# Kernel optimization log

Measured on AMD Instinct MI355X. Metric: run time of the kernel, lower is better.

## Reference

```python
import jax, jax.numpy as jnp
import numpy as np

B, N, D, H, DFF = 2, 2048, 1024, 16, 4096
HD = D // H
L = 3
WINDOWS = (256, 64, 16)   # sliding-window size per hierarchy level
LEVEL_SCALE = 16          # pos_l = token_idx // LEVEL_SCALE**l
EPS = 1e-5
NEG = -1e9


def setup_inputs() -> dict:
    key = jax.random.key(0)
    ks = jax.random.split(key, 16)
    s = 0.02
    x = jax.random.normal(ks[0], (B, N, D), dtype=jnp.float32)
    idx = jnp.arange(N, dtype=jnp.int32)
    positions = jnp.stack([idx // (LEVEL_SCALE ** l) for l in range(L)], axis=0)  # [L, N]
    return {
        "x": x,
        "positions": positions,
        "w_qkv": jax.random.normal(ks[1], (D, 3 * D), dtype=jnp.float32) * s,
        "b_qkv": jnp.zeros((3 * D,), dtype=jnp.float32),
        "w_out": jax.random.normal(ks[2], (D, D), dtype=jnp.float32) * s,
        "b_out": jnp.zeros((D,), dtype=jnp.float32),
        "w_ff1": jax.random.normal(ks[3], (D, DFF), dtype=jnp.float32) * s,
        "b_ff1": jnp.zeros((DFF,), dtype=jnp.float32),
        "w_ff2": jax.random.normal(ks[4], (DFF, D), dtype=jnp.float32) * s,
        "b_ff2": jnp.zeros((D,), dtype=jnp.float32),
        "g1": jnp.ones((D,), dtype=jnp.float32),
        "beta1": jnp.zeros((D,), dtype=jnp.float32),
        "g2": jnp.ones((D,), dtype=jnp.float32),
        "beta2": jnp.zeros((D,), dtype=jnp.float32),
    }


def _layernorm(x, g, b):
    m = jnp.mean(x, axis=-1, keepdims=True)
    v = jnp.var(x, axis=-1, keepdims=True)
    return (x - m) * jax.lax.rsqrt(v + EPS) * g + b


def _mlswa_mask(positions):
    # union over levels of per-level sliding windows: |pos_l[i]-pos_l[j]| < w_l
    allowed = jnp.zeros((N, N), dtype=bool)
    for l, w in enumerate(WINDOWS):
        p = positions[l]
        allowed = allowed | (jnp.abs(p[:, None] - p[None, :]) < w)
    return allowed  # [N, N]


def reference(x, positions, w_qkv, b_qkv, w_out, b_out,
              w_ff1, b_ff1, w_ff2, b_ff2, g1, beta1, g2, beta2):
    residual = x
    xn = _layernorm(x, g1, beta1)
    qkv = xn @ w_qkv + b_qkv                       # [B, N, 3D]
    qkv = qkv.reshape(B, N, 3, H, HD)
    q, k, v = qkv[:, :, 0], qkv[:, :, 1], qkv[:, :, 2]  # [B, N, H, HD]

    scale = 1.0 / np.sqrt(HD)
    scores = jnp.einsum('bihd,bjhd->bhij', q, k) * scale  # [B, H, N, N]
    allowed = _mlswa_mask(positions)
    scores = jnp.where(allowed[None, None], scores, NEG)
    attn = jax.nn.softmax(scores, axis=-1)
    out = jnp.einsum('bhij,bjhd->bihd', attn, v).reshape(B, N, D)
    out = out @ w_out + b_out
    x = residual + out

    residual = x
    xn = _layernorm(x, g2, beta2)
    ff = jax.nn.gelu(xn @ w_ff1 + b_ff1, approximate=False) @ w_ff2 + b_ff2
    return residual + ff
```

## Files before the change

kernel.cpp:

```cpp
#include <hip/hip_runtime.h>
#include <cstdint>
#include <cstddef>


using u16 = unsigned short;
using u32 = unsigned int;

typedef __attribute__((ext_vector_type(8)))  short bf16x8;
typedef __attribute__((ext_vector_type(4)))  float f32x4;
typedef __attribute__((ext_vector_type(16))) float f32x16;

#define DEV __device__ __forceinline__

DEV u16 f2bf(float f) {
  u32 u = __builtin_bit_cast(u32, f);
  u32 r = (u + 0x7FFFu + ((u >> 16) & 1u)) >> 16;
  return (u16)r;
}
DEV float bf2f(u16 u) { return __builtin_bit_cast(float, (u32)u << 16); }
DEV u32 pk2(float a, float b) { return (u32)f2bf(a) | ((u32)f2bf(b) << 16); }
DEV u32 cvtpk(float lo, float hi) {
  u32 r;
  asm("v_cvt_pk_bf16_f32 %0, %1, %2" : "=v"(r) : "v"(lo), "v"(hi));
  return r;
}
DEV float fexp2(float x) { return __builtin_amdgcn_exp2f(x); }

DEV void gload_lds16(const void* g, void* lds) {
  __builtin_amdgcn_global_load_lds(
      (const __attribute__((address_space(1))) u32*)g,
      (__attribute__((address_space(3))) u32*)lds, 16, 0, 0);
}

DEV float fast_gelu(float x) {
  float u = x * fmaf(0.035677408137f, x * x, 0.7978845608f);
  u = fminf(fmaxf(u, -15.0f), 15.0f);
  float e = fexp2(u * 2.885390081777927f);
  return x * e * __builtin_amdgcn_rcpf(e + 1.0f);
}

__global__ __launch_bounds__(256) void k_transpose_bf16(const float* __restrict__ in,
                                                        u16* __restrict__ out, int R, int C) {
  __shared__ float ts[32][33];
  int n0 = blockIdx.x * 32, r0 = blockIdx.y * 32;
  int t = threadIdx.x;
  int c = t & 31, r = t >> 5;
#pragma unroll
  for (int j = 0; j < 4; ++j)
    ts[r + 8 * j][c] = in[(size_t)(r0 + r + 8 * j) * C + n0 + c];
  __syncthreads();
#pragma unroll
  for (int j = 0; j < 4; ++j)
    out[(size_t)(n0 + r + 8 * j) * R + r0 + c] = f2bf(ts[c][r + 8 * j]);
}

__global__ __launch_bounds__(256) void k_layernorm(const float* __restrict__ x,
                                                   const float* __restrict__ g,
                                                   const float* __restrict__ be,
                                                   u16* __restrict__ o) {
  int row = blockIdx.x;
  int t = threadIdx.x;
  const float* xr = x + (size_t)row * 1024;
  f32x4 v = *(const f32x4*)(xr + t * 4);
  float s = v[0] + v[1] + v[2] + v[3];
  float s2 = v[0] * v[0] + v[1] * v[1] + v[2] * v[2] + v[3] * v[3];
#pragma unroll
  for (int off = 1; off < 64; off <<= 1) {
    s += __shfl_xor(s, off);
    s2 += __shfl_xor(s2, off);
  }
  __shared__ float red[8];
  if ((t & 63) == 0) { red[t >> 6] = s; red[4 + (t >> 6)] = s2; }
  __syncthreads();
  s = red[0] + red[1] + red[2] + red[3];
  s2 = red[4] + red[5] + red[6] + red[7];
  float mean = s * (1.0f / 1024.0f);
  float var = fmaxf(s2 * (1.0f / 1024.0f) - mean * mean, 0.0f);
  float rstd = rsqrtf(var + 1e-5f);
  f32x4 gg = *(const f32x4*)(g + t * 4);
  f32x4 bb = *(const f32x4*)(be + t * 4);
  uint2 ww;
  ww.x = pk2((v[0] - mean) * rstd * gg[0] + bb[0], (v[1] - mean) * rstd * gg[1] + bb[1]);
  ww.y = pk2((v[2] - mean) * rstd * gg[2] + bb[2], (v[3] - mean) * rstd * gg[3] + bb[3]);
  *(uint2*)(o + (size_t)row * 1024 + t * 4) = ww;
}

template <int MODE, int SPLIT>
__global__ __launch_bounds__(SPLIT * 256) void k_gemm(
    const u16* __restrict__ A, const u16* __restrict__ Bt, int K, int NC,
    const float* __restrict__ bias, const float* __restrict__ resid,
    void* __restrict__ o0, void* __restrict__ o1, void* __restrict__ o2) {
  __shared__ u16 tiles[SPLIT][2][128 * 64];
  const int lane = threadIdx.x & 63, wave = threadIdx.x >> 6;
  const int group = (SPLIT >= 2) ? (wave >> 2) : 0;
  const int wv = wave & 3;
  const int nwg = gridDim.x * gridDim.y;
  const int id = blockIdx.y * gridDim.x + blockIdx.x;
  const int wg = (id & 7) * (nwg >> 3) + (id >> 3);
  const int tN = (wg % gridDim.x) * 128, tM = (wg / gridDim.x) * 128;
  const int wm = (wv >> 1) * 64, wn = (wv & 1) * 64;
  const int lm = lane & 15, lh = lane >> 4;
  const int K2 = K / SPLIT;
  const int kbase = group * K2;
  f32x4 acc[4][4] = {};

  auto STAGE = [&](int k0) {
#pragma unroll
    for (int i = 0; i < 4; ++i) {
      int seg = i * 4 + wv;
      int li = seg * 64 + lane;
      int m = li >> 3, ch = li & 7;
      gload_lds16(A + (size_t)(tM + m) * K + kbase + k0 + ((ch ^ (m & 7)) << 3),
                  (void*)(tiles[group][0] + seg * 512));
      gload_lds16(Bt + (size_t)(tN + m) * K + kbase + k0 + ((ch ^ (m & 7)) << 3),
                  (void*)(tiles[group][1] + seg * 512));
    }
  };

  const int nk = K2 >> 6;
  for (int t = 0; t < nk; ++t) {
    __syncthreads();
    STAGE(t << 6);
    __syncthreads();
#pragma unroll
    for (int s = 0; s < 2; ++s) {
      bf16x8 af[4], bfr[4];
#pragma unroll
      for (int i = 0; i < 4; ++i) {
        int m = wm + i * 16 + lm;
        af[i] = *(const bf16x8*)((const char*)tiles[group][0] + m * 128 +
                                 (((s * 4 + lh) ^ (m & 7)) << 4));
      }
#pragma unroll
      for (int j = 0; j < 4; ++j) {
        int n = wn + j * 16 + lm;
        bfr[j] = *(const bf16x8*)((const char*)tiles[group][1] + n * 128 +
                                  (((s * 4 + lh) ^ (n & 7)) << 4));
      }
#pragma unroll
      for (int i = 0; i < 4; ++i)
#pragma unroll
        for (int j = 0; j < 4; ++j)
          acc[i][j] = __builtin_amdgcn_mfma_f32_16x16x32_bf16(af[i], bfr[j], acc[i][j], 0, 0, 0);
    }
  }

  auto dumpacc = [&](float* c) {
#pragma unroll
    for (int i = 0; i < 4; ++i)
#pragma unroll
      for (int j = 0; j < 4; ++j)
        *(f32x4*)&c[(i * 4 + j) * 1024 + wv * 256 + lane * 4] = acc[i][j];
  };
  auto addacc = [&](const float* c) {
#pragma unroll
    for (int i = 0; i < 4; ++i)
#pragma unroll
      for (int j = 0; j < 4; ++j) {
        f32x4 o4 = *(const f32x4*)&c[(i * 4 + j) * 1024 + wv * 256 + lane * 4];
#pragma unroll
        for (int r = 0; r < 4; ++r) acc[i][j][r] += o4[r];
      }
  };

  if constexpr (SPLIT == 4) {
    float* cA = (float*)&tiles[0][0][0];
    float* cB = (float*)&tiles[2][0][0];
    __syncthreads();
    if (group == 1) dumpacc(cA);
    if (group == 3) dumpacc(cB);
    __syncthreads();
    if (group == 0) addacc(cA);
    if (group == 2) addacc(cB);
    __syncthreads();
    if (group == 2) dumpacc(cA);
    __syncthreads();
    if (group == 0) { addacc(cA); dumpacc(cB); }
    __syncthreads();
    {
      const int i = group;
#pragma unroll
      for (int j = 0; j < 4; ++j) {
        int gn = tN + wn + j * 16 + lm;
        int gm0 = tM + wm + i * 16 + lh * 4;
        f32x4 v4 = *(const f32x4*)&cB[(i * 4 + j) * 1024 + wv * 256 + lane * 4];
        float bv = bias[gn];
#pragma unroll
        for (int r = 0; r < 4; ++r)
          ((float*)o0)[(size_t)(gm0 + r) * NC + gn] =
              v4[r] + bv + resid[(size_t)(gm0 + r) * NC + gn];
      }
    }
    return;
  }

  if constexpr (SPLIT == 2) {
    float* comb = (float*)tiles;
    __syncthreads();
    if (group == 1) dumpacc(comb);
    __syncthreads();
    if (group == 1) return;
    addacc(comb);
  }

#pragma unroll
  for (int i = 0; i < 4; ++i) {
#pragma unroll
    for (int j = 0; j < 4; ++j) {
      int gn = tN + wn + j * 16 + lm;
      int gm0 = tM + wm + i * 16 + lh * 4;
      float vals[4];
#pragma unroll
      for (int r = 0; r < 4; ++r) vals[r] = acc[i][j][r] + bias[gn];
      if constexpr (MODE == 0) {
        int which = gn >> 10, h = (gn >> 6) & 15, d = gn & 63;
        int b = gm0 >> 11, nn0 = gm0 & 2047;
        if (which == 2) {
          uint2 w2;
          w2.x = pk2(vals[0], vals[1]);
          w2.y = pk2(vals[2], vals[3]);
          *(uint2*)((u16*)o2 + ((size_t)(b * 16 + h) * 64 + d) * 2048 + nn0) = w2;
        } else {
          u16* dst = which == 0 ? (u16*)o0 : (u16*)o1;
          float sc = which == 0 ? 0.125f : 1.0f;
#pragma unroll
          for (int r = 0; r < 4; ++r)
            dst[(((size_t)(b * 16 + h)) * 2048 + nn0 + r) * 64 + d] = f2bf(vals[r] * sc);
        }
      } else if constexpr (MODE == 2) {
#pragma unroll
        for (int r = 0; r < 4; ++r)
          ((u16*)o0)[(size_t)(gm0 + r) * NC + gn] = f2bf(fast_gelu(vals[r]));
      } else {
#pragma unroll
        for (int r = 0; r < 4; ++r)
          ((float*)o0)[(size_t)(gm0 + r) * NC + gn] =
              vals[r] + resid[(size_t)(gm0 + r) * NC + gn];
      }
    }
  }
}

__global__ __launch_bounds__(256) void k_attn(const u16* __restrict__ q,
                                              const u16* __restrict__ k,
                                              const u16* __restrict__ vt,
                                              u16* __restrict__ o) {
  __shared__ u16 KT[2][4096];
  __shared__ u16 VT[2][4096];
  const int tid = threadIdx.x;
  const int lane = tid & 63, wave = tid >> 6;
  const int ql = lane & 31, hi = lane >> 5;
  const int id = blockIdx.y * 16 + blockIdx.x;
  const int wg = (id & 7) * 64 + (id >> 3);
  const int qb = wg & 15, bh = wg >> 4;
  const int q0 = qb * 128 + wave * 32;
  const float C_LOG2E = 1.44269504088896f;
  const float MSHIFT = 8.0f * C_LOG2E;

  const u16* qp = q + ((size_t)bh * 2048 + q0 + ql) * 64 + hi * 8;
  bf16x8 qf[4];
#pragma unroll
  for (int dc = 0; dc < 4; ++dc) qf[dc] = *(const bf16x8*)(qp + dc * 16);

  const u16* kst = k + (size_t)bh * 2048 * 64;
  const u16* vst = vt + (size_t)bh * 64 * 2048;

  f32x16 ot0 = {0, 0, 0, 0, 0, 0, 0, 0, 0, 0, 0, 0, 0, 0, 0, 0};
  f32x16 ot1 = ot0;
  float lsum = 0.0f;

  u32 koffA[4], koffB[4], voffA[4], voffB[4];
#pragma unroll
  for (int dc = 0; dc < 4; ++dc) {
    u32 sw = (((u32)((dc << 1) | hi) ^ (ql & 7)) << 3);
    koffA[dc] = (ql << 6) + sw;
    koffB[dc] = ((32 + ql) << 6) + sw;
  }
#pragma unroll
  for (int kc = 0; kc < 2; ++kc)
#pragma unroll
    for (int dh = 0; dh < 2; ++dh) {
      u32 rb = ((u32)((dh << 5) + ql) << 6);
      voffA[kc * 2 + dh] = rb + ((((kc << 1) + hi) ^ (ql & 7)) << 3);
      voffB[kc * 2 + dh] = rb + (((4 + (kc << 1) + hi) ^ (ql & 7)) << 3);
    }

  auto STAGE = [&](int tl, int b) {
    int kb = tl << 6;
#pragma unroll
    for (int i = 0; i < 2; ++i) {
      int seg = i * 4 + wave;
      int li = seg * 64 + lane;
      int row = li >> 3, ch = li & 7;
      int sw = (ch ^ (row & 7)) << 3;
      gload_lds16(kst + (size_t)(kb + row) * 64 + sw, (void*)&KT[b][seg * 512]);
      gload_lds16(vst + (size_t)row * 2048 + kb + sw, (void*)&VT[b][seg * 512]);
    }
  };

  auto COMPUTE = [&](const u16* KTb, const u16* VTb) {
    f32x16 st0 = {0, 0, 0, 0, 0, 0, 0, 0, 0, 0, 0, 0, 0, 0, 0, 0};
    f32x16 st1 = st0;
    bf16x8 kfa[4], kfb[4];
#pragma unroll
    for (int dc = 0; dc < 4; ++dc) {
      kfa[dc] = *(const bf16x8*)(KTb + koffA[dc]);
      kfb[dc] = *(const bf16x8*)(KTb + koffB[dc]);
    }
    __builtin_amdgcn_s_setprio(1);
#pragma unroll
    for (int dc = 0; dc < 4; ++dc) {
      st0 = __builtin_amdgcn_mfma_f32_32x32x16_bf16(kfa[dc], qf[dc], st0, 0, 0, 0);
      st1 = __builtin_amdgcn_mfma_f32_32x32x16_bf16(kfb[dc], qf[dc], st1, 0, 0, 0);
    }
    __builtin_amdgcn_s_setprio(0);
    bf16x8 vf0[4], vf1[4];
#pragma unroll
    for (int i = 0; i < 4; ++i) {
      vf0[i] = *(const bf16x8*)(VTb + voffA[i]);
      vf1[i] = *(const bf16x8*)(VTb + voffB[i]);
    }
    float p0[16], p1v[16];
#pragma unroll
    for (int r = 0; r < 16; ++r) {
      p0[r] = fexp2(fmaf(st0[r], C_LOG2E, -MSHIFT));
      p1v[r] = fexp2(fmaf(st1[r], C_LOG2E, -MSHIFT));
    }
    float s8[8];
#pragma unroll
    for (int r = 0; r < 8; ++r)
      s8[r] = (p0[2 * r] + p0[2 * r + 1]) + (p1v[2 * r] + p1v[2 * r + 1]);
#pragma unroll
    for (int r = 0; r < 4; ++r) s8[r] = s8[r] + s8[r + 4];
    float ts = (s8[0] + s8[2]) + (s8[1] + s8[3]);
    {
      float p1 = ts, p2 = ts;
      asm("v_permlane32_swap_b32 %0, %1" : "+v"(p1), "+v"(p2));
      ts = p1 + p2;
    }
    lsum += ts;
    __builtin_amdgcn_s_setprio(1);
#pragma unroll
    for (int kc = 0; kc < 2; ++kc) {
      u32 x0 = cvtpk(p0[kc * 8 + 0], p0[kc * 8 + 1]), x1 = cvtpk(p0[kc * 8 + 2], p0[kc * 8 + 3]);
      u32 y0 = cvtpk(p0[kc * 8 + 4], p0[kc * 8 + 5]), y1 = cvtpk(p0[kc * 8 + 6], p0[kc * 8 + 7]);
      asm("v_permlane32_swap_b32 %0, %1" : "+v"(x0), "+v"(y0));
      asm("v_permlane32_swap_b32 %0, %1" : "+v"(x1), "+v"(y1));
      union { u32 u[4]; bf16x8 v8; } pf;
      pf.u[0] = x0; pf.u[1] = x1; pf.u[2] = y0; pf.u[3] = y1;
      ot0 = __builtin_amdgcn_mfma_f32_32x32x16_bf16(vf0[kc * 2 + 0], pf.v8, ot0, 0, 0, 0);
      ot1 = __builtin_amdgcn_mfma_f32_32x32x16_bf16(vf0[kc * 2 + 1], pf.v8, ot1, 0, 0, 0);
    }
#pragma unroll
    for (int kc = 0; kc < 2; ++kc) {
      u32 x0 = cvtpk(p1v[kc * 8 + 0], p1v[kc * 8 + 1]), x1 = cvtpk(p1v[kc * 8 + 2], p1v[kc * 8 + 3]);
      u32 y0 = cvtpk(p1v[kc * 8 + 4], p1v[kc * 8 + 5]), y1 = cvtpk(p1v[kc * 8 + 6], p1v[kc * 8 + 7]);
      asm("v_permlane32_swap_b32 %0, %1" : "+v"(x0), "+v"(y0));
      asm("v_permlane32_swap_b32 %0, %1" : "+v"(x1), "+v"(y1));
      union { u32 u[4]; bf16x8 v8; } pf;
      pf.u[0] = x0; pf.u[1] = x1; pf.u[2] = y0; pf.u[3] = y1;
      ot0 = __builtin_amdgcn_mfma_f32_32x32x16_bf16(vf1[kc * 2 + 0], pf.v8, ot0, 0, 0, 0);
      ot1 = __builtin_amdgcn_mfma_f32_32x32x16_bf16(vf1[kc * 2 + 1], pf.v8, ot1, 0, 0, 0);
    }
    __builtin_amdgcn_s_setprio(0);
  };

  STAGE(0, 0);
  __syncthreads();

#pragma unroll 1
  for (int t2 = 0; t2 < 16; ++t2) {
    const int tlA = t2 * 2;
    STAGE(tlA + 1, 1);
    COMPUTE(KT[0], VT[0]);
    __syncthreads();
    if (t2 < 15) STAGE(tlA + 2, 0);
    COMPUTE(KT[1], VT[1]);
    __syncthreads();
  }

  float inv = 1.0f / lsum;
  int b = bh >> 4, h = bh & 15;
  size_t ob = ((size_t)b * 2048 + q0 + ql) * 1024 + h * 64;
#pragma unroll
  for (int r = 0; r < 16; ++r) {
    int d = (r & 3) + ((r >> 2) << 3) + hi * 4;
    o[ob + d] = f2bf(ot0[r] * inv);
    o[ob + 32 + d] = f2bf(ot1[r] * inv);
  }
}

extern "C" void kernel_launch(void* const* d_in, const int* in_sizes, int n_in,
                              void* d_out, int out_size, void* d_ws, size_t ws_size,
                              hipStream_t stream) {
  const float* x = (const float*)d_in[0];
  const float* w_qkv = (const float*)d_in[2];
  const float* b_qkv = (const float*)d_in[3];
  const float* w_out = (const float*)d_in[4];
  const float* b_out = (const float*)d_in[5];
  const float* w_ff1 = (const float*)d_in[6];
  const float* b_ff1 = (const float*)d_in[7];
  const float* w_ff2 = (const float*)d_in[8];
  const float* b_ff2 = (const float*)d_in[9];
  const float* g1 = (const float*)d_in[10];
  const float* be1 = (const float*)d_in[11];
  const float* g2 = (const float*)d_in[12];
  const float* be2 = (const float*)d_in[13];
  float* out = (float*)d_out;

  char* wp = (char*)d_ws;
  u16* wqkvT = (u16*)wp; wp += (size_t)3072 * 1024 * 2;
  u16* woutT = (u16*)wp; wp += (size_t)1024 * 1024 * 2;
  u16* wff1T = (u16*)wp; wp += (size_t)4096 * 1024 * 2;
  u16* wff2T = (u16*)wp; wp += (size_t)1024 * 4096 * 2;
  u16* xn    = (u16*)wp; wp += (size_t)4096 * 1024 * 2;
  float* x2  = (float*)wp; wp += (size_t)4096 * 1024 * 4;
  u16* qbuf  = (u16*)wp; wp += (size_t)32 * 2048 * 64 * 2;
  u16* kbuf  = (u16*)wp; wp += (size_t)32 * 2048 * 64 * 2;
  u16* vtbuf = (u16*)wp; wp += (size_t)32 * 2048 * 64 * 2;
  u16* attnb = (u16*)wp; wp += (size_t)4096 * 1024 * 2;
  u16* ffh   = qbuf;

  k_transpose_bf16<<<dim3(3072 / 32, 1024 / 32), 256, 0, stream>>>(w_qkv, wqkvT, 1024, 3072);
  k_transpose_bf16<<<dim3(1024 / 32, 1024 / 32), 256, 0, stream>>>(w_out, woutT, 1024, 1024);
  k_transpose_bf16<<<dim3(4096 / 32, 1024 / 32), 256, 0, stream>>>(w_ff1, wff1T, 1024, 4096);
  k_transpose_bf16<<<dim3(1024 / 32, 4096 / 32), 256, 0, stream>>>(w_ff2, wff2T, 4096, 1024);

  k_layernorm<<<4096, 256, 0, stream>>>(x, g1, be1, xn);
  k_gemm<0, 2><<<dim3(24, 32), 512, 0, stream>>>(xn, wqkvT, 1024, 3072, b_qkv, nullptr,
                                                 qbuf, kbuf, vtbuf);
  k_attn<<<dim3(16, 32), 256, 0, stream>>>(qbuf, kbuf, vtbuf, attnb);
  k_gemm<1, 2><<<dim3(8, 32), 512, 0, stream>>>(attnb, woutT, 1024, 1024, b_out, x,
                                                x2, nullptr, nullptr);
  k_layernorm<<<4096, 256, 0, stream>>>(x2, g2, be2, xn);
  k_gemm<2, 2><<<dim3(32, 32), 512, 0, stream>>>(xn, wff1T, 1024, 4096, b_ff1, nullptr,
                                                 ffh, nullptr, nullptr);
  k_gemm<3, 4><<<dim3(8, 32), 1024, 0, stream>>>(ffh, wff2T, 4096, 1024, b_ff2, x2,
                                                 out, nullptr, nullptr);
}
```

Before: 245.4 us.

## Split attention KV range across two workgroups and combine partials

```diff
diff --git a/kernel.cpp b/kernel.cpp
--- a/kernel.cpp
+++ b/kernel.cpp
@@ -244,15 +244,16 @@
 __global__ __launch_bounds__(256) void k_attn(const u16* __restrict__ q,
                                               const u16* __restrict__ k,
                                               const u16* __restrict__ vt,
-                                              u16* __restrict__ o) {
+                                              u16* __restrict__ pO,
+                                              float* __restrict__ pL) {
   __shared__ u16 KT[2][4096];
   __shared__ u16 VT[2][4096];
   const int tid = threadIdx.x;
   const int lane = tid & 63, wave = tid >> 6;
   const int ql = lane & 31, hi = lane >> 5;
-  const int id = blockIdx.y * 16 + blockIdx.x;
-  const int wg = (id & 7) * 64 + (id >> 3);
-  const int qb = wg & 15, bh = wg >> 4;
+  const int id = blockIdx.y * 32 + blockIdx.x;
+  const int wg = (id & 7) * 128 + (id >> 3);
+  const int split = wg & 1, qb = (wg >> 1) & 15, bh = wg >> 5;
   const int q0 = qb * 128 + wave * 32;
   const float C_LOG2E = 1.44269504088896f;
   const float MSHIFT = 8.0f * C_LOG2E;
@@ -262,8 +263,8 @@
 #pragma unroll
   for (int dc = 0; dc < 4; ++dc) qf[dc] = *(const bf16x8*)(qp + dc * 16);
 
-  const u16* kst = k + (size_t)bh * 2048 * 64;
-  const u16* vst = vt + (size_t)bh * 64 * 2048;
+  const u16* kst = k + ((size_t)bh * 2048 + split * 1024) * 64;
+  const u16* vst = vt + (size_t)bh * 64 * 2048 + split * 1024;
 
   f32x16 ot0 = {0, 0, 0, 0, 0, 0, 0, 0, 0, 0, 0, 0, 0, 0, 0, 0};
   f32x16 ot1 = ot0;
@@ -369,25 +370,44 @@
   __syncthreads();
 
 #pragma unroll 1
-  for (int t2 = 0; t2 < 16; ++t2) {
+  for (int t2 = 0; t2 < 8; ++t2) {
     const int tlA = t2 * 2;
     STAGE(tlA + 1, 1);
     COMPUTE(KT[0], VT[0]);
     __syncthreads();
-    if (t2 < 15) STAGE(tlA + 2, 0);
+    if (t2 < 7) STAGE(tlA + 2, 0);
     COMPUTE(KT[1], VT[1]);
     __syncthreads();
   }
 
-  float inv = 1.0f / lsum;
+  size_t pb = ((size_t)(bh * 2 + split) * 2048 + q0 + ql) * 64;
+#pragma unroll
+  for (int rr = 0; rr < 4; ++rr) {
+    int d0 = (rr << 3) + hi * 4;
+    uint2 wA, wB;
+    wA.x = cvtpk(ot0[rr * 4 + 0], ot0[rr * 4 + 1]);
+    wA.y = cvtpk(ot0[rr * 4 + 2], ot0[rr * 4 + 3]);
+    wB.x = cvtpk(ot1[rr * 4 + 0], ot1[rr * 4 + 1]);
+    wB.y = cvtpk(ot1[rr * 4 + 2], ot1[rr * 4 + 3]);
+    *(uint2*)(pO + pb + d0) = wA;
+    *(uint2*)(pO + pb + 32 + d0) = wB;
+  }
+  if (hi == 0) pL[(size_t)(bh * 2 + split) * 2048 + q0 + ql] = lsum;
+}
+
+__global__ __launch_bounds__(256) void k_combine(const u16* __restrict__ pO,
+                                                 const float* __restrict__ pL,
+                                                 u16* __restrict__ o) {
+  int t = threadIdx.x;
+  int row = blockIdx.x * 4 + (t >> 6);
+  int d = t & 63;
+  int bh = row >> 11, qq = row & 2047;
+  float L = pL[(size_t)(bh * 2 + 0) * 2048 + qq] + pL[(size_t)(bh * 2 + 1) * 2048 + qq];
+  float s0 = bf2f(pO[((size_t)(bh * 2 + 0) * 2048 + qq) * 64 + d]);
+  float s1 = bf2f(pO[((size_t)(bh * 2 + 1) * 2048 + qq) * 64 + d]);
+  float res = (s0 + s1) * __builtin_amdgcn_rcpf(L);
   int b = bh >> 4, h = bh & 15;
-  size_t ob = ((size_t)b * 2048 + q0 + ql) * 1024 + h * 64;
-#pragma unroll
-  for (int r = 0; r < 16; ++r) {
-    int d = (r & 3) + ((r >> 2) << 3) + hi * 4;
-    o[ob + d] = f2bf(ot0[r] * inv);
-    o[ob + 32 + d] = f2bf(ot1[r] * inv);
-  }
+  o[((size_t)(b * 2048 + qq)) * 1024 + h * 64 + d] = f2bf(res);
 }
 
 extern "C" void kernel_launch(void* const* d_in, const int* in_sizes, int n_in,
@@ -420,6 +440,8 @@
   u16* vtbuf = (u16*)wp; wp += (size_t)32 * 2048 * 64 * 2;
   u16* attnb = (u16*)wp; wp += (size_t)4096 * 1024 * 2;
   u16* ffh   = qbuf;
+  u16* pO = xn;
+  float* pL = (float*)((char*)xn + (17u << 20));
 
   k_transpose_bf16<<<dim3(3072 / 32, 1024 / 32), 256, 0, stream>>>(w_qkv, wqkvT, 1024, 3072);
   k_transpose_bf16<<<dim3(1024 / 32, 1024 / 32), 256, 0, stream>>>(w_out, woutT, 1024, 1024);
@@ -429,9 +451,10 @@
   k_layernorm<<<4096, 256, 0, stream>>>(x, g1, be1, xn);
   k_gemm<0, 2><<<dim3(24, 32), 512, 0, stream>>>(xn, wqkvT, 1024, 3072, b_qkv, nullptr,
                                                  qbuf, kbuf, vtbuf);
-  k_attn<<<dim3(16, 32), 256, 0, stream>>>(qbuf, kbuf, vtbuf, attnb);
-  k_gemm<1, 2><<<dim3(8, 32), 512, 0, stream>>>(attnb, woutT, 1024, 1024, b_out, x,
-                                                x2, nullptr, nullptr);
+  k_attn<<<dim3(32, 32), 256, 0, stream>>>(qbuf, kbuf, vtbuf, pO, pL);
+  k_combine<<<16384, 256, 0, stream>>>(pO, pL, attnb);
+  k_gemm<1, 4><<<dim3(8, 32), 1024, 0, stream>>>(attnb, woutT, 1024, 1024, b_out, x,
+                                                 x2, nullptr, nullptr);
   k_layernorm<<<4096, 256, 0, stream>>>(x2, g2, be2, xn);
   k_gemm<2, 2><<<dim3(32, 32), 512, 0, stream>>>(xn, wff1T, 1024, 4096, b_ff1, nullptr,
                                                  ffh, nullptr, nullptr);
```

After: 254.8 us. 3.8% more time.
